# Kernel tuning notes

Hardware: AMD Instinct MI355X
Metric: run time of the kernel (lower is better)

The kernel has to match this reference:

```python
import jax, jax.numpy as jnp
import numpy as np

WS = 8      # window size
NH = 8      # num heads


def setup_inputs() -> dict:
    key = jax.random.key(0)
    ks = jax.random.split(key, 5)
    B, H, W, C = 8, 250, 250, 256
    x = jax.random.normal(ks[0], (B, H * W, C), dtype=jnp.float32)
    qkv_w = jax.random.normal(ks[1], (3 * C, C), dtype=jnp.float32) * (C ** -0.5)
    proj_w = jax.random.normal(ks[2], (C, C), dtype=jnp.float32) * (C ** -0.5)
    proj_b = jax.random.normal(ks[3], (C,), dtype=jnp.float32) * 0.02
    rel_bias = jax.random.normal(ks[4], (NH, WS * WS, WS * WS), dtype=jnp.float32) * 0.02
    return {"x": x, "qkv_w": qkv_w, "proj_w": proj_w, "proj_b": proj_b,
            "rel_bias": rel_bias, "H": H, "W": W}


def reference(x, qkv_w, proj_w, proj_b, rel_bias, H, W):
    B, L, C = x.shape
    hd = C // NH
    scale = hd ** -0.5
    ws2 = WS * WS

    pad_b = (WS - H % WS) % WS
    pad_r = (WS - W % WS) % WS
    Hp, Wp = H + pad_b, W + pad_r

    xi = x.reshape(B, H, W, C)
    xi = jnp.pad(xi, ((0, 0), (0, pad_b), (0, pad_r), (0, 0)))
    # window partition -> [B*nWh*nWw, ws*ws, C]
    xi = xi.reshape(B, Hp // WS, WS, Wp // WS, WS, C)
    windows = xi.transpose(0, 1, 3, 2, 4, 5).reshape(-1, ws2, C)

    # qkv projection (no bias): Linear weight layout [out, in]
    qkv = windows @ qkv_w.T                              # [nW, ws2, 3C]
    qkv = qkv.reshape(-1, ws2, 3, NH, hd).transpose(2, 0, 3, 1, 4)  # [3, nW, nh, ws2, hd]
    q, k, v = qkv[0], qkv[1], qkv[2]

    attn = jnp.einsum('whqd,whkd->whqk', q * scale, k) + rel_bias[None]
    attn = jax.nn.softmax(attn, axis=-1)
    out = jnp.einsum('whqk,whkd->whqd', attn, v)          # [nW, nh, ws2, hd]
    out = out.transpose(0, 2, 1, 3).reshape(-1, ws2, C)
    out = out @ proj_w.T + proj_b

    # window merge and crop back to [B, H*W, C]
    out = out.reshape(B, Hp // WS, Wp // WS, WS, WS, C)
    out = out.transpose(0, 1, 3, 2, 4, 5).reshape(B, Hp, Wp, C)
    out = out[:, :H, :W, :]
    return out.reshape(B, H * W, C)
```

## Files before the change

### kernel.cpp

```cpp
#include <hip/hip_runtime.h>
#include <hip/hip_bf16.h>

typedef short bf16x8 __attribute__((ext_vector_type(8)));
typedef float f32x4 __attribute__((ext_vector_type(4)));

#define MFMA16(A,B,C) __builtin_amdgcn_mfma_f32_16x16x32_bf16(A,B,C,0,0,0)
#define PRIO_HI() __builtin_amdgcn_s_setprio(1)
#define PRIO_LO() __builtin_amdgcn_s_setprio(0)

static __device__ __forceinline__ unsigned short f2bf(float f) {
  __hip_bfloat16 h = __float2bfloat16(f);
  unsigned short u; __builtin_memcpy(&u, &h, 2); return u;
}
static __device__ __forceinline__ ushort4 pack4(f32x4 v) {
  ushort4 p; p.x = f2bf(v[0]); p.y = f2bf(v[1]); p.z = f2bf(v[2]); p.w = f2bf(v[3]);
  return p;
}

#define SWZ(row, byte) ((byte) ^ (((row) & 7) << 4))

#define OFF_XW 0
#define OFF_QK 32768
#define OFF_VT 49152
#define OFF_P  57344
#define OFF_O4 73728
#define LDS_TOTAL 81920

#define NQKV 196608
#define NPROJ 65536

__global__ void convert_w_kernel(const float* __restrict__ qkv_w,
                                 const float* __restrict__ proj_w,
                                 ushort* __restrict__ wsb) {
  int i = blockIdx.x * 256 + threadIdx.x;
  if (i < NQKV) {
    float v = qkv_w[i];
    if (i < 65536) v *= 0.17677669529663687f;
    wsb[i] = f2bf(v);
  } else if (i < NQKV + NPROJ) {
    wsb[i] = f2bf(proj_w[i - NQKV]);
  }
}

__global__ __launch_bounds__(512, 2)
void swin_fused_pair(const float* __restrict__ x,
                     const ushort* __restrict__ qkvw,
                     const ushort* __restrict__ projw,
                     const float* __restrict__ proj_b,
                     const float* __restrict__ rel_bias,
                     float* __restrict__ out) {
  extern __shared__ char smem[];

  const int wid = blockIdx.x;
  const int bb_ = wid >> 10;
  const int wy  = (wid >> 5) & 31;
  const int wx  = wid & 31;
  const int tid  = threadIdx.x;
  const int wave = tid >> 6;
  const int lane = tid & 63;
  const int l16  = lane & 15;
  const int lq   = lane >> 4;

  #pragma unroll
  for (int it = 0; it < 8; ++it) {
    const int t  = it * 8 + wave;
    const int gr = wy * 8 + (t >> 3);
    const int gc = wx * 8 + (t & 7);
    float4 v = make_float4(0.f, 0.f, 0.f, 0.f);
    if (gr < 250 && gc < 250)
      v = *(const float4*)(x + ((size_t)bb_ * 62500 + (size_t)gr * 250 + gc) * 256 + lane * 4);
    ushort4 bv;
    bv.x = f2bf(v.x); bv.y = f2bf(v.y); bv.z = f2bf(v.z); bv.w = f2bf(v.w);
    *(ushort4*)(smem + OFF_XW + t * 512 + SWZ(t, lane * 8)) = bv;
  }

  f32x4 oacc[4][2];
  #pragma unroll
  for (int m = 0; m < 4; ++m)
    #pragma unroll
    for (int n = 0; n < 2; ++n)
      oacc[m][n] = f32x4{0.f, 0.f, 0.f, 0.f};

  const int hl2 = wave >> 2;
  const int r0  = (wave & 3) * 16;

  #pragma unroll 1
  for (int pass = 0; pass < 4; ++pass) {
    __syncthreads();

    if (pass > 0) {
      PRIO_HI();
      #pragma unroll
      for (int kk = 0; kk < 2; ++kk) {
        bf16x8 af[4];
        #pragma unroll
        for (int m = 0; m < 4; ++m) {
          const int r = m * 16 + l16;
          af[m] = *(const bf16x8*)(smem + OFF_O4 + r * 128 + SWZ(r, kk * 64 + lq * 16));
        }
        #pragma unroll
        for (int nt = 0; nt < 2; ++nt) {
          const int c = wave * 32 + nt * 16 + l16;
          bf16x8 bfr = *(const bf16x8*)(projw + (size_t)c * 256 + (pass - 1) * 64 + kk * 32 + lq * 8);
          #pragma unroll
          for (int m = 0; m < 4; ++m)
            oacc[m][nt] = MFMA16(af[m], bfr, oacc[m][nt]);
        }
      }
      PRIO_LO();
    }

    if (wave < 4) {
      const int head = wave >> 1, dhalf = wave & 1;
      #pragma unroll 1
      for (int ty = 0; ty < 2; ++ty) {
        const int wrow = ty * 256 + (pass * 2 + head) * 32 + dhalf * 16 + l16;
        const ushort* wp = qkvw + (size_t)wrow * 256 + lq * 8;
        f32x4 acc[4];
        #pragma unroll
        for (int n = 0; n < 4; ++n) acc[n] = f32x4{0.f, 0.f, 0.f, 0.f};
        PRIO_HI();
        #pragma unroll 2
        for (int kk = 0; kk < 8; ++kk) {
          bf16x8 wf = *(const bf16x8*)(wp + kk * 32);
          #pragma unroll
          for (int n = 0; n < 4; ++n) {
            const int t = n * 16 + l16;
            bf16x8 xf = *(const bf16x8*)(smem + OFF_XW + t * 512 + SWZ(t, kk * 64 + lq * 16));
            acc[n] = MFMA16(wf, xf, acc[n]);
          }
        }
        PRIO_LO();
        const int dby = ty * 64 + dhalf * 32 + lq * 8;
        #pragma unroll
        for (int n = 0; n < 4; ++n) {
          const int t = n * 16 + l16;
          *(ushort4*)(smem + OFF_QK + (head * 64 + t) * 128 + SWZ(t, dby)) = pack4(acc[n]);
        }
      }
    } else {
      const int head = (wave - 4) >> 1, dhalf = (wave - 4) & 1;
      const int wrow = 512 + (pass * 2 + head) * 32 + dhalf * 16 + l16;
      const ushort* wp = qkvw + (size_t)wrow * 256 + lq * 8;
      f32x4 acc[4];
      #pragma unroll
      for (int m = 0; m < 4; ++m) acc[m] = f32x4{0.f, 0.f, 0.f, 0.f};
      PRIO_HI();
      #pragma unroll 2
      for (int kk = 0; kk < 8; ++kk) {
        bf16x8 wf = *(const bf16x8*)(wp + kk * 32);
        #pragma unroll
        for (int m = 0; m < 4; ++m) {
          const int t = m * 16 + l16;
          bf16x8 xf = *(const bf16x8*)(smem + OFF_XW + t * 512 + SWZ(t, kk * 64 + lq * 16));
          acc[m] = MFMA16(xf, wf, acc[m]);
        }
      }
      PRIO_LO();
      const int d = dhalf * 16 + l16;
      #pragma unroll
      for (int m = 0; m < 4; ++m)
        *(ushort4*)(smem + OFF_VT + (head * 32 + d) * 128 + SWZ(d, (m * 16 + lq * 4) * 2)) = pack4(acc[m]);
    }
    __syncthreads();

    f32x4 s[4];
    {
      const int qr_ = r0 + l16;
      bf16x8 qf = *(const bf16x8*)(smem + OFF_QK + (hl2 * 64 + qr_) * 128 + SWZ(qr_, lq * 16));
      PRIO_HI();
      #pragma unroll
      for (int m = 0; m < 4; ++m) {
        const int kt = m * 16 + l16;
        bf16x8 kf = *(const bf16x8*)(smem + OFF_QK + (hl2 * 64 + kt) * 128 + SWZ(kt, 64 + lq * 16));
        s[m] = MFMA16(kf, qf, (f32x4{0.f, 0.f, 0.f, 0.f}));
      }
      PRIO_LO();
    }

    const float* biasb = rel_bias + (size_t)(pass * 2 + hl2) * 4096 + (size_t)(r0 + l16) * 64;
    float ssum = 0.f;
    const int qr = r0 + l16;
    #pragma unroll
    for (int m = 0; m < 4; ++m) {
      const float4 bv = *(const float4*)(biasb + m * 16 + lq * 4);
      f32x4 e;
      e[0] = __expf(s[m][0] + bv.x);
      e[1] = __expf(s[m][1] + bv.y);
      e[2] = __expf(s[m][2] + bv.z);
      e[3] = __expf(s[m][3] + bv.w);
      ssum += (e[0] + e[1]) + (e[2] + e[3]);
      *(ushort4*)(smem + OFF_P + (hl2 * 64 + qr) * 128 + SWZ(qr, m * 32 + lq * 8)) = pack4(e);
    }
    ssum += __shfl_xor(ssum, 16);
    ssum += __shfl_xor(ssum, 32);
    const float rcp = 1.f / ssum;

    f32x4 o[2];
    o[0] = f32x4{0.f, 0.f, 0.f, 0.f};
    o[1] = f32x4{0.f, 0.f, 0.f, 0.f};
    PRIO_HI();
    #pragma unroll
    for (int kk = 0; kk < 2; ++kk) {
      bf16x8 pf = *(const bf16x8*)(smem + OFF_P + (hl2 * 64 + qr) * 128 + SWZ(qr, kk * 64 + lq * 16));
      #pragma unroll
      for (int mt = 0; mt < 2; ++mt) {
        const int d = mt * 16 + l16;
        bf16x8 vf = *(const bf16x8*)(smem + OFF_VT + (hl2 * 32 + d) * 128 + SWZ(d, kk * 64 + lq * 16));
        o[mt] = MFMA16(vf, pf, o[mt]);
      }
    }
    PRIO_LO();
    #pragma unroll
    for (int mt = 0; mt < 2; ++mt) {
      f32x4 sc;
      sc[0] = o[mt][0] * rcp; sc[1] = o[mt][1] * rcp;
      sc[2] = o[mt][2] * rcp; sc[3] = o[mt][3] * rcp;
      *(ushort4*)(smem + OFF_O4 + qr * 128 + SWZ(qr, hl2 * 64 + mt * 32 + lq * 8)) = pack4(sc);
    }
  }

  __syncthreads();
  PRIO_HI();
  #pragma unroll
  for (int kk = 0; kk < 2; ++kk) {
    bf16x8 af[4];
    #pragma unroll
    for (int m = 0; m < 4; ++m) {
      const int r = m * 16 + l16;
      af[m] = *(const bf16x8*)(smem + OFF_O4 + r * 128 + SWZ(r, kk * 64 + lq * 16));
    }
    #pragma unroll
    for (int nt = 0; nt < 2; ++nt) {
      const int c = wave * 32 + nt * 16 + l16;
      bf16x8 bfr = *(const bf16x8*)(projw + (size_t)c * 256 + 3 * 64 + kk * 32 + lq * 8);
      #pragma unroll
      for (int m = 0; m < 4; ++m)
        oacc[m][nt] = MFMA16(af[m], bfr, oacc[m][nt]);
    }
  }
  PRIO_LO();
  __syncthreads();
  #pragma unroll
  for (int nt = 0; nt < 2; ++nt) {
    const int col = wave * 32 + nt * 16 + l16;
    const float pb = proj_b[col];
    #pragma unroll
    for (int m = 0; m < 4; ++m)
      #pragma unroll
      for (int rr = 0; rr < 4; ++rr) {
        const int row = m * 16 + lq * 4 + rr;
        *(float*)(smem + row * 1024 + SWZ(row, col * 4)) = oacc[m][nt][rr] + pb;
      }
  }
  __syncthreads();
  #pragma unroll
  for (int it = 0; it < 8; ++it) {
    const int t  = it * 8 + wave;
    const int gr = wy * 8 + (t >> 3);
    const int gc = wx * 8 + (t & 7);
    if (gr < 250 && gc < 250) {
      float4 v = *(const float4*)(smem + t * 1024 + SWZ(t, lane * 16));
      *(float4*)(out + ((size_t)bb_ * 62500 + (size_t)gr * 250 + gc) * 256 + lane * 4) = v;
    }
  }
}

extern "C" void kernel_launch(void* const* d_in, const int* in_sizes, int n_in,
                              void* d_out, int out_size, void* d_ws, size_t ws_size,
                              hipStream_t stream) {
  const float* x        = (const float*)d_in[0];
  const float* qkv_w    = (const float*)d_in[1];
  const float* proj_w   = (const float*)d_in[2];
  const float* proj_b   = (const float*)d_in[3];
  const float* rel_bias = (const float*)d_in[4];
  float* out = (float*)d_out;
  ushort* wsb = (ushort*)d_ws;

  (void)in_sizes; (void)n_in; (void)out_size; (void)ws_size;

  hipFuncSetAttribute((const void*)swin_fused_pair,
                      hipFuncAttributeMaxDynamicSharedMemorySize, LDS_TOTAL);

  convert_w_kernel<<<1024, 256, 0, stream>>>(qkv_w, proj_w, wsb);
  swin_fused_pair<<<8192, 512, LDS_TOTAL, stream>>>(x, wsb, wsb + NQKV, proj_b,
                                                    rel_bias, out);
}
```

Measured before the change: 741.6 us.

## Use 1024-thread blocks, redistribute QKV/attention/proj waves, fold log2e and bias into MFMA

Doubles the block to 16 waves at one block per CU. The Q/K projection now runs on eight waves, so the two-iteration ty loop is gone. V runs on four waves and attention on eight. The output projection is split across all 16 waves at 16 columns each. The softmax uses exp2f with log2e folded into the pre-scaled Q weights and into a pre-scaled copy of rel_bias in the workspace, and that bias seeds the QK^T MFMA accumulator. This shortens the per-pass critical path and removes the adds before exp. The cost is larger, costlier block-wide barriers, fewer independent blocks to overlap, and four waves idle during attention.

```diff
diff --git a/kernel.cpp b/kernel.cpp
--- a/kernel.cpp
+++ b/kernel.cpp
@@ -28,26 +28,31 @@
 
 #define NQKV 196608
 #define NPROJ 65536
+#define NBIAS 32768
+#define LOG2E 1.4426950408889634f
 
 __global__ void convert_w_kernel(const float* __restrict__ qkv_w,
                                  const float* __restrict__ proj_w,
+                                 const float* __restrict__ rel_bias,
                                  ushort* __restrict__ wsb) {
   int i = blockIdx.x * 256 + threadIdx.x;
   if (i < NQKV) {
     float v = qkv_w[i];
-    if (i < 65536) v *= 0.17677669529663687f;
+    if (i < 65536) v *= 0.17677669529663687f * LOG2E;
     wsb[i] = f2bf(v);
   } else if (i < NQKV + NPROJ) {
     wsb[i] = f2bf(proj_w[i - NQKV]);
-  }
-}
-
-__global__ __launch_bounds__(512, 2)
+  } else if (i < NQKV + NPROJ + NBIAS) {
+    ((float*)(wsb + NQKV + NPROJ))[i - NQKV - NPROJ] = rel_bias[i - NQKV - NPROJ] * LOG2E;
+  }
+}
+
+__global__ __launch_bounds__(1024, 1)
 void swin_fused_pair(const float* __restrict__ x,
                      const ushort* __restrict__ qkvw,
                      const ushort* __restrict__ projw,
                      const float* __restrict__ proj_b,
-                     const float* __restrict__ rel_bias,
+                     const float* __restrict__ biasw,
                      float* __restrict__ out) {
   extern __shared__ char smem[];
 
@@ -62,8 +67,8 @@
   const int lq   = lane >> 4;
 
   #pragma unroll
-  for (int it = 0; it < 8; ++it) {
-    const int t  = it * 8 + wave;
+  for (int it = 0; it < 4; ++it) {
+    const int t  = it * 16 + wave;
     const int gr = wy * 8 + (t >> 3);
     const int gc = wx * 8 + (t & 7);
     float4 v = make_float4(0.f, 0.f, 0.f, 0.f);
@@ -74,15 +79,14 @@
     *(ushort4*)(smem + OFF_XW + t * 512 + SWZ(t, lane * 8)) = bv;
   }
 
-  f32x4 oacc[4][2];
-  #pragma unroll
-  for (int m = 0; m < 4; ++m)
-    #pragma unroll
-    for (int n = 0; n < 2; ++n)
-      oacc[m][n] = f32x4{0.f, 0.f, 0.f, 0.f};
-
-  const int hl2 = wave >> 2;
-  const int r0  = (wave & 3) * 16;
+  f32x4 oacc[4];
+  #pragma unroll
+  for (int m = 0; m < 4; ++m) oacc[m] = f32x4{0.f, 0.f, 0.f, 0.f};
+
+  const bool spv = (wave >= 12) || (wave >= 4 && wave < 8);
+  const int slot = (wave >= 12) ? (wave - 12) + 4 : (wave - 4);
+  const int hl2 = (slot >> 2) & 1;
+  const int r0  = (slot & 3) * 16;
 
   #pragma unroll 1
   for (int pass = 0; pass < 4; ++pass) {
@@ -98,48 +102,43 @@
           const int r = m * 16 + l16;
           af[m] = *(const bf16x8*)(smem + OFF_O4 + r * 128 + SWZ(r, kk * 64 + lq * 16));
         }
-        #pragma unroll
-        for (int nt = 0; nt < 2; ++nt) {
-          const int c = wave * 32 + nt * 16 + l16;
-          bf16x8 bfr = *(const bf16x8*)(projw + (size_t)c * 256 + (pass - 1) * 64 + kk * 32 + lq * 8);
-          #pragma unroll
-          for (int m = 0; m < 4; ++m)
-            oacc[m][nt] = MFMA16(af[m], bfr, oacc[m][nt]);
-        }
-      }
-      PRIO_LO();
-    }
-
-    if (wave < 4) {
-      const int head = wave >> 1, dhalf = wave & 1;
-      #pragma unroll 1
-      for (int ty = 0; ty < 2; ++ty) {
-        const int wrow = ty * 256 + (pass * 2 + head) * 32 + dhalf * 16 + l16;
-        const ushort* wp = qkvw + (size_t)wrow * 256 + lq * 8;
-        f32x4 acc[4];
-        #pragma unroll
-        for (int n = 0; n < 4; ++n) acc[n] = f32x4{0.f, 0.f, 0.f, 0.f};
-        PRIO_HI();
-        #pragma unroll 2
-        for (int kk = 0; kk < 8; ++kk) {
-          bf16x8 wf = *(const bf16x8*)(wp + kk * 32);
-          #pragma unroll
-          for (int n = 0; n < 4; ++n) {
-            const int t = n * 16 + l16;
-            bf16x8 xf = *(const bf16x8*)(smem + OFF_XW + t * 512 + SWZ(t, kk * 64 + lq * 16));
-            acc[n] = MFMA16(wf, xf, acc[n]);
-          }
-        }
-        PRIO_LO();
-        const int dby = ty * 64 + dhalf * 32 + lq * 8;
+        const int c = wave * 16 + l16;
+        bf16x8 bfr = *(const bf16x8*)(projw + (size_t)c * 256 + (pass - 1) * 64 + kk * 32 + lq * 8);
+        #pragma unroll
+        for (int m = 0; m < 4; ++m)
+          oacc[m] = MFMA16(af[m], bfr, oacc[m]);
+      }
+      PRIO_LO();
+    }
+
+    if (wave < 8) {
+      const int ty = wave >> 2;
+      const int head = (wave >> 1) & 1, dhalf = wave & 1;
+      const int wrow = ty * 256 + (pass * 2 + head) * 32 + dhalf * 16 + l16;
+      const ushort* wp = qkvw + (size_t)wrow * 256 + lq * 8;
+      f32x4 acc[4];
+      #pragma unroll
+      for (int n = 0; n < 4; ++n) acc[n] = f32x4{0.f, 0.f, 0.f, 0.f};
+      PRIO_HI();
+      #pragma unroll 2
+      for (int kk = 0; kk < 8; ++kk) {
+        bf16x8 wf = *(const bf16x8*)(wp + kk * 32);
         #pragma unroll
         for (int n = 0; n < 4; ++n) {
           const int t = n * 16 + l16;
-          *(ushort4*)(smem + OFF_QK + (head * 64 + t) * 128 + SWZ(t, dby)) = pack4(acc[n]);
-        }
-      }
-    } else {
-      const int head = (wave - 4) >> 1, dhalf = (wave - 4) & 1;
+          bf16x8 xf = *(const bf16x8*)(smem + OFF_XW + t * 512 + SWZ(t, kk * 64 + lq * 16));
+          acc[n] = MFMA16(wf, xf, acc[n]);
+        }
+      }
+      PRIO_LO();
+      const int dby = ty * 64 + dhalf * 32 + lq * 8;
+      #pragma unroll
+      for (int n = 0; n < 4; ++n) {
+        const int t = n * 16 + l16;
+        *(ushort4*)(smem + OFF_QK + (head * 64 + t) * 128 + SWZ(t, dby)) = pack4(acc[n]);
+      }
+    } else if (wave < 12) {
+      const int head = (wave >> 1) & 1, dhalf = wave & 1;
       const int wrow = 512 + (pass * 2 + head) * 32 + dhalf * 16 + l16;
       const ushort* wp = qkvw + (size_t)wrow * 256 + lq * 8;
       f32x4 acc[4];
@@ -164,59 +163,61 @@
     }
     __syncthreads();
 
-    f32x4 s[4];
-    {
-      const int qr_ = r0 + l16;
-      bf16x8 qf = *(const bf16x8*)(smem + OFF_QK + (hl2 * 64 + qr_) * 128 + SWZ(qr_, lq * 16));
-      PRIO_HI();
+    if (spv) {
+      const int qr = r0 + l16;
+      const float* biasb = biasw + (size_t)(pass * 2 + hl2) * 4096 + (size_t)qr * 64;
+
+      f32x4 s[4];
+      {
+        bf16x8 qf = *(const bf16x8*)(smem + OFF_QK + (hl2 * 64 + qr) * 128 + SWZ(qr, lq * 16));
+        PRIO_HI();
+        #pragma unroll
+        for (int m = 0; m < 4; ++m) {
+          const int kt = m * 16 + l16;
+          bf16x8 kf = *(const bf16x8*)(smem + OFF_QK + (hl2 * 64 + kt) * 128 + SWZ(kt, 64 + lq * 16));
+          f32x4 bi = *(const f32x4*)(biasb + m * 16 + lq * 4);
+          s[m] = MFMA16(kf, qf, bi);
+        }
+        PRIO_LO();
+      }
+
+      float ssum = 0.f;
       #pragma unroll
       for (int m = 0; m < 4; ++m) {
-        const int kt = m * 16 + l16;
-        bf16x8 kf = *(const bf16x8*)(smem + OFF_QK + (hl2 * 64 + kt) * 128 + SWZ(kt, 64 + lq * 16));
-        s[m] = MFMA16(kf, qf, (f32x4{0.f, 0.f, 0.f, 0.f}));
-      }
-      PRIO_LO();
-    }
-
-    const float* biasb = rel_bias + (size_t)(pass * 2 + hl2) * 4096 + (size_t)(r0 + l16) * 64;
-    float ssum = 0.f;
-    const int qr = r0 + l16;
-    #pragma unroll
-    for (int m = 0; m < 4; ++m) {
-      const float4 bv = *(const float4*)(biasb + m * 16 + lq * 4);
-      f32x4 e;
-      e[0] = __expf(s[m][0] + bv.x);
-      e[1] = __expf(s[m][1] + bv.y);
-      e[2] = __expf(s[m][2] + bv.z);
-      e[3] = __expf(s[m][3] + bv.w);
-      ssum += (e[0] + e[1]) + (e[2] + e[3]);
-      *(ushort4*)(smem + OFF_P + (hl2 * 64 + qr) * 128 + SWZ(qr, m * 32 + lq * 8)) = pack4(e);
-    }
-    ssum += __shfl_xor(ssum, 16);
-    ssum += __shfl_xor(ssum, 32);
-    const float rcp = 1.f / ssum;
-
-    f32x4 o[2];
-    o[0] = f32x4{0.f, 0.f, 0.f, 0.f};
-    o[1] = f32x4{0.f, 0.f, 0.f, 0.f};
-    PRIO_HI();
-    #pragma unroll
-    for (int kk = 0; kk < 2; ++kk) {
-      bf16x8 pf = *(const bf16x8*)(smem + OFF_P + (hl2 * 64 + qr) * 128 + SWZ(qr, kk * 64 + lq * 16));
+        f32x4 e;
+        e[0] = exp2f(s[m][0]);
+        e[1] = exp2f(s[m][1]);
+        e[2] = exp2f(s[m][2]);
+        e[3] = exp2f(s[m][3]);
+        ssum += (e[0] + e[1]) + (e[2] + e[3]);
+        *(ushort4*)(smem + OFF_P + (hl2 * 64 + qr) * 128 + SWZ(qr, m * 32 + lq * 8)) = pack4(e);
+      }
+      ssum += __shfl_xor(ssum, 16);
+      ssum += __shfl_xor(ssum, 32);
+      const float rcp = 1.f / ssum;
+
+      f32x4 o[2];
+      o[0] = f32x4{0.f, 0.f, 0.f, 0.f};
+      o[1] = f32x4{0.f, 0.f, 0.f, 0.f};
+      PRIO_HI();
+      #pragma unroll
+      for (int kk = 0; kk < 2; ++kk) {
+        bf16x8 pf = *(const bf16x8*)(smem + OFF_P + (hl2 * 64 + qr) * 128 + SWZ(qr, kk * 64 + lq * 16));
+        #pragma unroll
+        for (int mt = 0; mt < 2; ++mt) {
+          const int d = mt * 16 + l16;
+          bf16x8 vf = *(const bf16x8*)(smem + OFF_VT + (hl2 * 32 + d) * 128 + SWZ(d, kk * 64 + lq * 16));
+          o[mt] = MFMA16(vf, pf, o[mt]);
+        }
+      }
+      PRIO_LO();
       #pragma unroll
       for (int mt = 0; mt < 2; ++mt) {
-        const int d = mt * 16 + l16;
-        bf16x8 vf = *(const bf16x8*)(smem + OFF_VT + (hl2 * 32 + d) * 128 + SWZ(d, kk * 64 + lq * 16));
-        o[mt] = MFMA16(vf, pf, o[mt]);
-      }
-    }
-    PRIO_LO();
-    #pragma unroll
-    for (int mt = 0; mt < 2; ++mt) {
-      f32x4 sc;
-      sc[0] = o[mt][0] * rcp; sc[1] = o[mt][1] * rcp;
-      sc[2] = o[mt][2] * rcp; sc[3] = o[mt][3] * rcp;
-      *(ushort4*)(smem + OFF_O4 + qr * 128 + SWZ(qr, hl2 * 64 + mt * 32 + lq * 8)) = pack4(sc);
+        f32x4 sc;
+        sc[0] = o[mt][0] * rcp; sc[1] = o[mt][1] * rcp;
+        sc[2] = o[mt][2] * rcp; sc[3] = o[mt][3] * rcp;
+        *(ushort4*)(smem + OFF_O4 + qr * 128 + SWZ(qr, hl2 * 64 + mt * 32 + lq * 8)) = pack4(sc);
+      }
     }
   }
 
@@ -230,33 +231,28 @@
       const int r = m * 16 + l16;
       af[m] = *(const bf16x8*)(smem + OFF_O4 + r * 128 + SWZ(r, kk * 64 + lq * 16));
     }
+    const int c = wave * 16 + l16;
+    bf16x8 bfr = *(const bf16x8*)(projw + (size_t)c * 256 + 3 * 64 + kk * 32 + lq * 8);
     #pragma unroll
-    for (int nt = 0; nt < 2; ++nt) {
-      const int c = wave * 32 + nt * 16 + l16;
-      bf16x8 bfr = *(const bf16x8*)(projw + (size_t)c * 256 + 3 * 64 + kk * 32 + lq * 8);
-      #pragma unroll
-      for (int m = 0; m < 4; ++m)
-        oacc[m][nt] = MFMA16(af[m], bfr, oacc[m][nt]);
-    }
+    for (int m = 0; m < 4; ++m)
+      oacc[m] = MFMA16(af[m], bfr, oacc[m]);
   }
   PRIO_LO();
-  __syncthreads();
-  #pragma unroll
-  for (int nt = 0; nt < 2; ++nt) {
-    const int col = wave * 32 + nt * 16 + l16;
+  {
+    const int col = wave * 16 + l16;
     const float pb = proj_b[col];
     #pragma unroll
     for (int m = 0; m < 4; ++m)
       #pragma unroll
       for (int rr = 0; rr < 4; ++rr) {
         const int row = m * 16 + lq * 4 + rr;
-        *(float*)(smem + row * 1024 + SWZ(row, col * 4)) = oacc[m][nt][rr] + pb;
+        *(float*)(smem + row * 1024 + SWZ(row, col * 4)) = oacc[m][rr] + pb;
       }
   }
   __syncthreads();
   #pragma unroll
-  for (int it = 0; it < 8; ++it) {
-    const int t  = it * 8 + wave;
+  for (int it = 0; it < 4; ++it) {
+    const int t  = it * 16 + wave;
     const int gr = wy * 8 + (t >> 3);
     const int gc = wx * 8 + (t & 7);
     if (gr < 250 && gc < 250) {
@@ -282,7 +278,7 @@
   hipFuncSetAttribute((const void*)swin_fused_pair,
                       hipFuncAttributeMaxDynamicSharedMemorySize, LDS_TOTAL);
 
-  convert_w_kernel<<<1024, 256, 0, stream>>>(qkv_w, proj_w, wsb);
-  swin_fused_pair<<<8192, 512, LDS_TOTAL, stream>>>(x, wsb, wsb + NQKV, proj_b,
-                                                    rel_bias, out);
-}
+  convert_w_kernel<<<1152, 256, 0, stream>>>(qkv_w, proj_w, rel_bias, wsb);
+  swin_fused_pair<<<8192, 1024, LDS_TOTAL, stream>>>(
+      x, wsb, wsb + NQKV, proj_b, (const float*)(wsb + NQKV + NPROJ), out);
+}
```

Result: slower. 914.7 us (+23.4%).
